# Performance work log

Hardware: AMD Instinct MI355X
Metric: run time of the kernel (lower is better)

## Reference

```python
import math
import jax, jax.numpy as jnp
import numpy as np

# dims (match init_kwargs)
N, K = 10000, 32            # nodes, padded neighbors per node
IN_F, H, HEADS = 128, 128, 8
T_F, R_F, OUT, LAYERS = 64, 32, 64, 2
HD = H // HEADS
START_T, END_T = 0.25, 0.75
ATTN_NORM = math.sqrt(1.0 / HD)
T_NORM = math.sqrt(1.0 / (T_F // 2))
EPS = 1e-5


def layernorm(x, g, b):
    m = jnp.mean(x, axis=-1, keepdims=True)
    v = jnp.var(x, axis=-1, keepdims=True)
    return (x - m) * jax.lax.rsqrt(v + EPS) * g + b


def t2v(dt, Wt, bt):
    # TimeKernel: linear(1->T_F/2) then interleaved [sin, cos] * norm
    h = dt[..., None] * Wt + bt                      # [..., T_F/2]
    return jnp.stack([jnp.sin(h), jnp.cos(h)], axis=-1).reshape(*h.shape[:-1], T_F) * T_NORM


def tgat_layer(x, neighbors, times, rels, mask,
               Wkqv, Wt, bt, Wtime, Wedge, g1, b1n, g2, b2n, W1, bl1, W2, bl2):
    xn = layernorm(x, g1, b1n)
    kqv = xn @ Wkqv                                  # [N, 3H], chunk order (k, q, v)
    k_, q_, v_ = jnp.split(kqv, 3, axis=1)
    kn = k_[neighbors]                               # [N, K, H] irregular gather
    vn = v_[neighbors]
    # per-node time reference: max over [start_t; masked times] (times>=start_t so start_t covered)
    tmax = jnp.max(jnp.where(mask, times, START_T), axis=1)        # [N]
    tq_emb = t2v(tmax - START_T, Wt, bt)             # [N, T_F] (the prepended start_t row)
    tn_emb = t2v(tmax[:, None] - times, Wt, bt)      # [N, K, T_F]
    t_qq = (tq_emb @ Wtime)[:, H:2 * H]              # query chunk of time KQV
    tkn = tn_emb @ Wtime                             # [N, K, 3H]
    re = rels @ Wedge                                # [N, K, 3H]
    q = q_ + t_qq                                    # [N, H]
    k = kn + tkn[..., :H] + re[..., :H]
    v = vn + tkn[..., 2 * H:] + re[..., 2 * H:]
    qh = q.reshape(N, HEADS, HD)
    kh = k.reshape(N, K, HEADS, HD)
    vh = v.reshape(N, K, HEADS, HD)
    scores = jnp.einsum('nhd,nkhd->nhk', qh, kh) * ATTN_NORM
    scores = jnp.where(mask[:, None, :], scores, -1e30)
    attn = jax.nn.softmax(scores, axis=-1)
    out = jnp.einsum('nhk,nkhd->nhd', attn, vh).reshape(N, H)
    has = jnp.any(mask, axis=1)                      # nodes with zero valid neighbors -> zeros
    h = jnp.where(has[:, None], out, 0.0)
    h2 = h + xn
    hn = layernorm(h2, g2, b2n)
    z = jnp.concatenate([xn, hn], axis=1)
    z = jax.nn.relu(z @ W1 + bl1) @ W2 + bl2
    return z + h2


def setup_inputs() -> dict:
    key = jax.random.key(0)
    ks = jax.random.split(key, 16)
    w = lambda i, *shape: jax.random.normal(ks[i], shape, dtype=jnp.float32) * 0.05
    return {
        'x': jax.random.normal(ks[0], (N, IN_F), dtype=jnp.float32),
        'neighbors': jax.random.randint(ks[1], (N, K), 0, N, dtype=jnp.int32),
        'times': jax.random.uniform(ks[2], (N, K), dtype=jnp.float32),
        'rels': jax.random.normal(ks[3], (N, K, R_F), dtype=jnp.float32),
        'Wp': w(4, IN_F, H), 'bp': jnp.zeros((H,), jnp.float32),
        'Wkqv': w(5, H, 3 * H),
        'Wt': w(6, T_F // 2), 'bt': jnp.zeros((T_F // 2,), jnp.float32),
        'Wtime': w(7, T_F, 3 * H),
        'Wedge': w(8, R_F, 3 * H),
        'g1': jnp.ones((H,), jnp.float32), 'b1n': jnp.zeros((H,), jnp.float32),
        'g2': jnp.ones((H,), jnp.float32), 'b2n': jnp.zeros((H,), jnp.float32),
        'W1': w(9, 2 * H, H), 'bl1': jnp.zeros((H,), jnp.float32),
        'W2': w(10, H, H), 'bl2': jnp.zeros((H,), jnp.float32),
        'Wo': w(11, H, OUT), 'bo': jnp.zeros((OUT,), jnp.float32),
    }


def reference(x, neighbors, times, rels, Wp, bp, Wkqv, Wt, bt, Wtime, Wedge,
              g1, b1n, g2, b2n, W1, bl1, W2, bl2, Wo, bo):
    mask = (times >= START_T) & (times < END_T)      # [N, K] temporal neighbor mask
    h = jax.nn.relu(x @ Wp + bp)
    for _ in range(LAYERS):                          # layers SHARE weights (ModuleList([layer]*layers))
        h = tgat_layer(h, neighbors, times, rels, mask,
                       Wkqv, Wt, bt, Wtime, Wedge, g1, b1n, g2, b2n, W1, bl1, W2, bl2)
    return h @ Wo + bo
```

## Files before the change

kernel.cpp:

```cpp
#include <hip/hip_runtime.h>
#include <hip/hip_bf16.h>

#define NN 10000
#define KK 32
#define HH 128
#define TFH 32
#define RFE 32
#define OUTF 64
#define START_T 0.25f
#define END_T 0.75f
#define ATTN_NORM 0.25f
#define T_NORM 0.17677669529663687f
#define LN_EPS 1e-5f
#define MT 64

typedef __attribute__((ext_vector_type(4))) float f32x4;
typedef __attribute__((ext_vector_type(8))) short bf16x8;

__device__ __forceinline__ ushort f2bf(float x){
  __hip_bfloat16 b = __float2bfloat16(x);
  return *(ushort*)&b;
}
__device__ __forceinline__ float bf2f(ushort u){
  __hip_bfloat16 b = *(__hip_bfloat16*)&u;
  return __bfloat162float(b);
}

__device__ __forceinline__ float groupsum32(float v){
  v += __shfl_xor(v, 16, 32);
  v += __shfl_xor(v, 8, 32);
  v += __shfl_xor(v, 4, 32);
  v += __shfl_xor(v, 2, 32);
  v += __shfl_xor(v, 1, 32);
  return v;
}

__device__ __forceinline__ float wavesum64(float v){
  v += __shfl_xor(v, 32, 64);
  v += __shfl_xor(v, 16, 64);
  v += __shfl_xor(v, 8, 64);
  v += __shfl_xor(v, 4, 64);
  v += __shfl_xor(v, 2, 64);
  v += __shfl_xor(v, 1, 64);
  return v;
}

__global__ __launch_bounds__(256) void k_prep_wT(const float* __restrict__ Wp, const float* __restrict__ Wkqv,
    const float* __restrict__ W1, const float* __restrict__ W2, const float* __restrict__ Wo,
    const float* __restrict__ Wtime, const float* __restrict__ Wedge,
    ushort* __restrict__ WpT, ushort* __restrict__ WkqvT, ushort* __restrict__ W1T,
    ushort* __restrict__ W2T, ushort* __restrict__ WoT, ushort* __restrict__ WcT){
  int id = blockIdx.x*256 + threadIdx.x;
  if (id < 16384){ int n=id>>7, k=id&127; WpT[id]=f2bf(Wp[k*HH+n]); return; }
  id -= 16384;
  if (id < 49152){ int n=id>>7, k=id&127; WkqvT[id]=f2bf(Wkqv[k*384+n]); return; }
  id -= 49152;
  if (id < 32768){ int n=id>>8, k=id&255; W1T[id]=f2bf(W1[k*HH+n]); return; }
  id -= 32768;
  if (id < 16384){ int n=id>>7, k=id&127; W2T[id]=f2bf(W2[k*HH+n]); return; }
  id -= 16384;
  if (id < 8192){ int n=id>>7, k=id&127; WoT[id]=f2bf(Wo[k*OUTF+n]); return; }
  id -= 8192;
  if (id < 24576){
    const int c = id/96, r = id%96;
    const int cc = (c < 128) ? c : (c + 128);
    const float v = (r < 64) ? Wtime[r*384 + cc] : Wedge[(r-64)*384 + cc];
    WcT[c*96 + r] = f2bf(v);
  }
}

#define LDA1 136
__global__ __launch_bounds__(256) void k_proj_mfma(const float* __restrict__ X, const ushort* __restrict__ WpT,
                                                   const float* __restrict__ bp, float* __restrict__ Y){
  __shared__ ushort As[16*LDA1];
  const int tid = threadIdx.x, n0 = blockIdx.x*16;
  #pragma unroll
  for (int p=0;p<2;++p){
    const int idx = tid + p*256;
    const int row = idx>>5, c4 = (idx&31)*4;
    const float4 v = *(const float4*)&X[(size_t)(n0+row)*HH + c4];
    *(ushort4*)&As[row*LDA1 + c4] = make_ushort4(f2bf(v.x), f2bf(v.y), f2bf(v.z), f2bf(v.w));
  }
  __syncthreads();
  const int w = tid>>6, lane = tid&63;
  const int lr = lane&15, lk8 = (lane>>4)*8, rbase = (lane>>4)*4;
  bf16x8 a[4];
  #pragma unroll
  for (int kk=0;kk<4;kk++) a[kk] = *(const bf16x8*)&As[lr*LDA1 + kk*32 + lk8];
  f32x4 acc[2];
  #pragma unroll
  for (int nt=0;nt<2;nt++) acc[nt] = (f32x4){0.f,0.f,0.f,0.f};
  #pragma unroll
  for (int nt=0;nt<2;nt++){
    const int n = w*2 + nt;
    #pragma unroll
    for (int kk=0;kk<4;kk++){
      bf16x8 b = *(const bf16x8*)&WpT[(n*16+lr)*HH + kk*32 + lk8];
      acc[nt] = __builtin_amdgcn_mfma_f32_16x16x32_bf16(a[kk], b, acc[nt],0,0,0);
    }
  }
  #pragma unroll
  for (int nt=0;nt<2;nt++){
    const int c = (w*2+nt)*16 + lr;
    const float bj = bp[c];
    #pragma unroll
    for (int r=0;r<4;r++)
      Y[(size_t)(n0 + rbase + r)*HH + c] = fmaxf(acc[nt][r] + bj, 0.f);
  }
}

__global__ __launch_bounds__(128) void k_prep_node(const float* __restrict__ times, const float* __restrict__ Wt,
                                                   const float* __restrict__ bt, const float* __restrict__ Wtime,
                                                   const int* __restrict__ nbrs,
                                                   float* __restrict__ tqq, float* __restrict__ tmaxb,
                                                   int* __restrict__ cntb, uint* __restrict__ vmaskb,
                                                   int* __restrict__ nbrC){
  __shared__ float temb[2*TFH];
  __shared__ float tm_sh;
  const int n = blockIdx.x, j = threadIdx.x;
  if (j < KK){
    float t = times[n*KK + j];
    bool valid = (t >= START_T) && (t < END_T);
    float val = valid ? t : START_T;
    #pragma unroll
    for (int off=16; off; off>>=1) val = fmaxf(val, __shfl_xor(val, off, 32));
    if (j==0){ tm_sh = val; tmaxb[n] = val; }
    const uint vm = (uint)__ballot(valid);
    if (valid){
      const int slot = __popc(vm & ((1u<<j)-1));
      nbrC[n*KK + slot] = nbrs[n*KK + j];
    }
    if (j==0){ cntb[n] = __popc(vm); vmaskb[n] = vm; }
  }
  __syncthreads();
  if (j < TFH){
    float hh = fmaf(tm_sh - START_T, Wt[j], bt[j]);
    temb[2*j]   = __sinf(hh)*T_NORM;
    temb[2*j+1] = __cosf(hh)*T_NORM;
  }
  __syncthreads();
  float acc = 0.f;
  #pragma unroll
  for (int f=0; f<2*TFH; f++) acc = fmaf(temb[f], Wtime[f*384 + HH + j], acc);
  tqq[n*HH + j] = acc;
}

#define LDA 104
#define LDKV 264
__global__ __launch_bounds__(256) void k_prep_kv4(
    const float* __restrict__ times, const float* __restrict__ rels, const float* __restrict__ tmaxb,
    const float* __restrict__ Wt, const float* __restrict__ bt, const ushort* __restrict__ WcT,
    const uint* __restrict__ vmaskb, uint4* __restrict__ kvout){
  __shared__ ushort smem[MT*LDKV];
  __shared__ float dt_sh[MT];
  ushort* Fa = smem;
  ushort* kvs = smem;
  const int tid = threadIdx.x;
  const int node0 = blockIdx.x*2;
  if (tid < MT){
    const int node = node0 + (tid>>5);
    dt_sh[tid] = tmaxb[node] - times[node*KK + (tid&31)];
  }
  __syncthreads();
  #pragma unroll
  for (int s0=0; s0<8; ++s0){
    const int s = tid + s0*256;
    const int p = s>>5, f = s&31;
    const float hh = fmaf(dt_sh[p], Wt[f], bt[f]);
    ushort2 pk;
    pk.x = f2bf(__sinf(hh)*T_NORM);
    pk.y = f2bf(__cosf(hh)*T_NORM);
    *(ushort2*)&Fa[p*LDA + 2*f] = pk;
  }
  #pragma unroll
  for (int s0=0; s0<2; ++s0){
    const int i = tid + s0*256;
    const int p = i>>3, seg = i&7;
    const float4 rv = *(const float4*)&rels[((size_t)node0*KK + p)*RFE + seg*4];
    ushort4 w2; w2.x=f2bf(rv.x); w2.y=f2bf(rv.y); w2.z=f2bf(rv.z); w2.w=f2bf(rv.w);
    *(ushort4*)&Fa[p*LDA + 64 + seg*4] = w2;
  }
  __syncthreads();
  const int wave = tid>>6, lane = tid&63;
  const int lr = lane&15, lk = (lane>>4)*8;
  f32x4 acc[4][4];
  #pragma unroll
  for (int m=0;m<4;m++)
    #pragma unroll
    for (int n=0;n<4;n++) acc[m][n] = (f32x4){0.f,0.f,0.f,0.f};
  #pragma unroll
  for (int kk=0; kk<3; ++kk){
    const int k0 = kk*32;
    bf16x8 a[4], b[4];
    #pragma unroll
    for (int m=0;m<4;m++) a[m] = *(const bf16x8*)&Fa[(m*16 + lr)*LDA + k0 + lk];
    #pragma unroll
    for (int n=0;n<4;n++) b[n] = *(const bf16x8*)&WcT[(wave*64 + n*16 + lr)*96 + k0 + lk];
    #pragma unroll
    for (int m=0;m<4;m++)
      #pragma unroll
      for (int n=0;n<4;n++)
        acc[m][n] = __builtin_amdgcn_mfma_f32_16x16x32_bf16(a[m], b[n], acc[m][n], 0,0,0);
  }
  __syncthreads();
  const int rbase = (lane>>4)*4;
  #pragma unroll
  for (int n=0;n<4;n++){
    const int c = wave*64 + n*16 + lr;
    const int ip = (c < 128) ? (2*c) : (2*(c-128)+1);
    #pragma unroll
    for (int m=0;m<4;m++)
      #pragma unroll
      for (int r=0;r<4;r++)
        kvs[(m*16 + rbase + r)*LDKV + ip] = f2bf(acc[m][n][r]);
  }
  __syncthreads();
  const uint vm0 = vmaskb[node0], vm1 = vmaskb[node0+1];
  #pragma unroll
  for (int pass=0; pass<8; ++pass){
    const int idx = pass*256 + tid;
    const int row = idx>>5, seg = idx&31;
    const int nloc = row>>5, k = row&31;
    const uint vm = nloc ? vm1 : vm0;
    if ((vm>>k)&1u){
      const int slot = __popc(vm & ((1u<<k)-1));
      const uint4 v = *(const uint4*)&kvs[row*LDKV + seg*8];
      kvout[((size_t)(node0+nloc)*KK + slot)*32 + seg] = v;
    }
  }
}

__global__ __launch_bounds__(256) void k_ln_kqv_mfma(const float* __restrict__ Hin, const ushort* __restrict__ WkqvT,
    const float* __restrict__ g1, const float* __restrict__ b1, const float* __restrict__ tqq,
    float* __restrict__ XN, ushort* __restrict__ xnb,
    float* __restrict__ Qf, ushort* __restrict__ KVb){
  __shared__ ushort As[16*LDA1];
  const int tid = threadIdx.x, n0 = blockIdx.x*16;
  const int grp = tid>>5, gl = tid&31;
  {
    const float4 gv = *(const float4*)&g1[gl*4];
    const float4 bv = *(const float4*)&b1[gl*4];
    #pragma unroll
    for (int rr=0; rr<2; ++rr){
      const int row = grp + rr*8;
      const int node = n0 + row;
      float4 hv = *(const float4*)&Hin[(size_t)node*HH + gl*4];
      float s = hv.x+hv.y+hv.z+hv.w;
      s = groupsum32(s);
      const float mean = s*(1.f/HH);
      const float dx=hv.x-mean, dy=hv.y-mean, dz=hv.z-mean, dw=hv.w-mean;
      float vs = dx*dx+dy*dy+dz*dz+dw*dw;
      vs = groupsum32(vs);
      const float rstd = rsqrtf(vs*(1.f/HH)+LN_EPS);
      const float x0=dx*rstd*gv.x+bv.x, x1=dy*rstd*gv.y+bv.y, x2=dz*rstd*gv.z+bv.z, x3=dw*rstd*gv.w+bv.w;
      ushort4 pk = make_ushort4(f2bf(x0), f2bf(x1), f2bf(x2), f2bf(x3));
      *(ushort4*)&As[row*LDA1 + gl*4] = pk;
      *(float4*)&XN[(size_t)node*HH + gl*4] = make_float4(x0,x1,x2,x3);
      *(ushort4*)&xnb[(size_t)node*HH + gl*4] = pk;
    }
  }
  __syncthreads();
  const int w = tid>>6, lane = tid&63;
  const int lr = lane&15, lk8 = (lane>>4)*8, rbase = (lane>>4)*4;
  bf16x8 a[4];
  #pragma unroll
  for (int kk=0;kk<4;kk++) a[kk] = *(const bf16x8*)&As[lr*LDA1 + kk*32 + lk8];
  f32x4 acc[6];
  #pragma unroll
  for (int nt=0;nt<6;nt++) acc[nt] = (f32x4){0.f,0.f,0.f,0.f};
  #pragma unroll
  for (int nt=0;nt<6;nt++){
    const int n = w*6 + nt;
    #pragma unroll
    for (int kk=0;kk<4;kk++){
      bf16x8 b = *(const bf16x8*)&WkqvT[(n*16+lr)*HH + kk*32 + lk8];
      acc[nt] = __builtin_amdgcn_mfma_f32_16x16x32_bf16(a[kk], b, acc[nt],0,0,0);
    }
  }
  #pragma unroll
  for (int nt=0;nt<6;nt++){
    const int c = (w*6+nt)*16 + lr;
    #pragma unroll
    for (int r=0;r<4;r++){
      const int node = n0 + rbase + r;
      const float v = acc[nt][r];
      if (c < HH)           KVb[(size_t)node*256 + 2*c] = f2bf(v);
      else if (c < 2*HH)    Qf[(size_t)node*HH + (c-HH)] = v + tqq[(size_t)node*HH + (c-HH)];
      else                  KVb[(size_t)node*256 + 2*(c-2*HH) + 1] = f2bf(v);
    }
  }
}

__global__ __launch_bounds__(256) void k_attn6(
    const float* __restrict__ Qf, const uint2* __restrict__ KVu2, const uint2* __restrict__ kvaddC2,
    const int* __restrict__ nbrC, const int* __restrict__ cntb,
    const float* __restrict__ XN, const float* __restrict__ g2, const float* __restrict__ b2,
    float* __restrict__ H2, ushort* __restrict__ hnb){
  __shared__ int nbr_sh[4][KK];
  const int tid = threadIdx.x, node0 = blockIdx.x*4;
  if (tid < 128) nbr_sh[tid>>5][tid&31] = nbrC[(node0 + (tid>>5))*KK + (tid&31)];
  __syncthreads();
  const int wv = tid>>6, l = tid&63;
  const int node = node0 + wv;
  const int cnt = cntb[node];
  const float2 q2 = *(const float2*)&Qf[(size_t)node*HH + 2*l];
  const float q0s = q2.x * ATTN_NORM, q1s = q2.y * ATTN_NORM;
  const uint2* karow = kvaddC2 + (size_t)node*KK*64 + l;
  float m_ = -3.0e38f, sume = 0.f, a0 = 0.f, a1 = 0.f;
  const int cc = (cnt + 7) >> 3;
  for (int ch=0; ch<cc; ++ch){
    const int base = ch*8;
    uint2 ka[8], kb[8];
    #pragma unroll
    for (int i=0;i<8;i++){
      int slot = base + i; slot = (slot < cnt) ? slot : (cnt-1);
      ka[i] = karow[(size_t)slot*64];
      kb[i] = KVu2[(size_t)nbr_sh[wv][slot]*64 + l];
    }
    float s[8];
    #pragma unroll
    for (int i=0;i<8;i++){
      float p = q0s * (bf2f((ushort)(kb[i].x&0xffff)) + bf2f((ushort)(ka[i].x&0xffff)))
              + q1s * (bf2f((ushort)(kb[i].y&0xffff)) + bf2f((ushort)(ka[i].y&0xffff)));
      p += __shfl_xor(p, 4, 8);
      p += __shfl_xor(p, 2, 8);
      p += __shfl_xor(p, 1, 8);
      s[i] = (base + i < cnt) ? p : -1e30f;
    }
    float cm = s[0];
    #pragma unroll
    for (int i=1;i<8;i++) cm = fmaxf(cm, s[i]);
    const float mn = fmaxf(m_, cm);
    const float sc = __expf(m_ - mn);
    sume *= sc; a0 *= sc; a1 *= sc;
    #pragma unroll
    for (int i=0;i<8;i++){
      const float e = __expf(s[i] - mn);
      sume += e;
      a0 = fmaf(e, bf2f((ushort)(kb[i].x>>16)) + bf2f((ushort)(ka[i].x>>16)), a0);
      a1 = fmaf(e, bf2f((ushort)(kb[i].y>>16)) + bf2f((ushort)(ka[i].y>>16)), a1);
    }
    m_ = mn;
  }
  const float inv = (cnt > 0) ? (1.f / sume) : 0.f;
  const float2 xn2 = *(const float2*)&XN[(size_t)node*HH + 2*l];
  const float h0 = a0*inv + xn2.x;
  const float h1 = a1*inv + xn2.y;
  *(float2*)&H2[(size_t)node*HH + 2*l] = make_float2(h0, h1);
  const float mean = wavesum64(h0 + h1) * (1.f/HH);
  const float d0 = h0 - mean, d1 = h1 - mean;
  const float var = wavesum64(d0*d0 + d1*d1) * (1.f/HH);
  const float rstd = rsqrtf(var + LN_EPS);
  const float2 gv = *(const float2*)&g2[2*l];
  const float2 bv = *(const float2*)&b2[2*l];
  ushort2 hn;
  hn.x = f2bf(d0*rstd*gv.x + bv.x);
  hn.y = f2bf(d1*rstd*gv.y + bv.y);
  *(ushort2*)&hnb[(size_t)node*HH + 2*l] = hn;
}

#define LDA2 264
template<int LAST>
__global__ __launch_bounds__(256) void k_ffn_mfma(const ushort* __restrict__ xnb, const ushort* __restrict__ hnb,
    const float* __restrict__ H2, const ushort* __restrict__ W1T, const float* __restrict__ bl1,
    const ushort* __restrict__ W2T, const float* __restrict__ bl2, float* __restrict__ HOUT,
    const ushort* __restrict__ WoT, const float* __restrict__ bo, float* __restrict__ OUT){
  __shared__ ushort As[16*LDA2];
  __shared__ ushort Ms[16*LDA1];
  const int tid = threadIdx.x, n0 = blockIdx.x*16;
  {
    const int row = tid>>4, c8 = (tid&15)*8;
    *(uint4*)&As[row*LDA2 + c8]       = *(const uint4*)&xnb[(size_t)(n0+row)*HH + c8];
    *(uint4*)&As[row*LDA2 + 128 + c8] = *(const uint4*)&hnb[(size_t)(n0+row)*HH + c8];
  }
  __syncthreads();
  const int w = tid>>6, lane = tid&63;
  const int lr = lane&15, lk8 = (lane>>4)*8, rbase = (lane>>4)*4;
  {
    bf16x8 a[8];
    #pragma unroll
    for (int kk=0;kk<8;kk++) a[kk] = *(const bf16x8*)&As[lr*LDA2 + kk*32 + lk8];
    f32x4 acc[2];
    #pragma unroll
    for (int nt=0;nt<2;nt++) acc[nt] = (f32x4){0.f,0.f,0.f,0.f};
    #pragma unroll
    for (int nt=0;nt<2;nt++){
      const int n = w*2 + nt;
      #pragma unroll
      for (int kk=0;kk<8;kk++){
        bf16x8 b = *(const bf16x8*)&W1T[(n*16+lr)*256 + kk*32 + lk8];
        acc[nt] = __builtin_amdgcn_mfma_f32_16x16x32_bf16(a[kk], b, acc[nt],0,0,0);
      }
    }
    #pragma unroll
    for (int nt=0;nt<2;nt++){
      const int c = (w*2+nt)*16 + lr;
      const float bj = bl1[c];
      #pragma unroll
      for (int r=0;r<4;r++)
        Ms[(rbase+r)*LDA1 + c] = f2bf(fmaxf(acc[nt][r] + bj, 0.f));
    }
  }
  __syncthreads();
  {
    bf16x8 a[4];
    #pragma unroll
    for (int kk=0;kk<4;kk++) a[kk] = *(const bf16x8*)&Ms[lr*LDA1 + kk*32 + lk8];
    f32x4 acc[2];
    #pragma unroll
    for (int nt=0;nt<2;nt++) acc[nt] = (f32x4){0.f,0.f,0.f,0.f};
    #pragma unroll
    for (int nt=0;nt<2;nt++){
      const int n = w*2 + nt;
      #pragma unroll
      for (int kk=0;kk<4;kk++){
        bf16x8 b = *(const bf16x8*)&W2T[(n*16+lr)*HH + kk*32 + lk8];
        acc[nt] = __builtin_amdgcn_mfma_f32_16x16x32_bf16(a[kk], b, acc[nt],0,0,0);
      }
    }
    #pragma unroll
    for (int nt=0;nt<2;nt++){
      const int c = (w*2+nt)*16 + lr;
      const float bj = bl2[c];
      #pragma unroll
      for (int r=0;r<4;r++){
        const size_t node = n0 + rbase + r;
        const float hout = acc[nt][r] + bj + H2[node*HH + c];
        if (LAST){
          ((ushort*)As)[(rbase+r)*LDA1 + c] = f2bf(hout);
        } else {
          HOUT[node*HH + c] = hout;
        }
      }
    }
  }
  if (LAST){
    __syncthreads();
    bf16x8 a[4];
    #pragma unroll
    for (int kk=0;kk<4;kk++) a[kk] = *(const bf16x8*)&((ushort*)As)[lr*LDA1 + kk*32 + lk8];
    f32x4 acc = (f32x4){0.f,0.f,0.f,0.f};
    #pragma unroll
    for (int kk=0;kk<4;kk++){
      bf16x8 b = *(const bf16x8*)&WoT[(w*16+lr)*HH + kk*32 + lk8];
      acc = __builtin_amdgcn_mfma_f32_16x16x32_bf16(a[kk], b, acc,0,0,0);
    }
    const int c = w*16 + lr;
    const float bj = bo[c];
    #pragma unroll
    for (int r=0;r<4;r++)
      OUT[(size_t)(n0 + rbase + r)*OUTF + c] = acc[r] + bj;
  }
}

extern "C" void kernel_launch(void* const* d_in, const int* in_sizes, int n_in,
                              void* d_out, int out_size, void* d_ws, size_t ws_size,
                              hipStream_t stream){
  const float* x         = (const float*)d_in[0];
  const int*   neighbors = (const int*)  d_in[1];
  const float* times     = (const float*)d_in[2];
  const float* rels      = (const float*)d_in[3];
  const float* Wp        = (const float*)d_in[4];
  const float* bp        = (const float*)d_in[5];
  const float* Wkqv      = (const float*)d_in[6];
  const float* Wt        = (const float*)d_in[7];
  const float* bt        = (const float*)d_in[8];
  const float* Wtime     = (const float*)d_in[9];
  const float* Wedge     = (const float*)d_in[10];
  const float* g1        = (const float*)d_in[11];
  const float* b1n       = (const float*)d_in[12];
  const float* g2        = (const float*)d_in[13];
  const float* b2n       = (const float*)d_in[14];
  const float* W1        = (const float*)d_in[15];
  const float* bl1       = (const float*)d_in[16];
  const float* W2        = (const float*)d_in[17];
  const float* bl2       = (const float*)d_in[18];
  const float* Wo        = (const float*)d_in[19];
  const float* bo        = (const float*)d_in[20];
  float* out = (float*)d_out;

  char* ws = (char*)d_ws;
  size_t off = 0;
  auto carve = [&](size_t bytes)->char*{
    char* p = ws + off; off = (off + bytes + 255) & ~(size_t)255; return p;
  };
  float* hA    = (float*)carve((size_t)NN*HH*4);
  float* hB    = (float*)carve((size_t)NN*HH*4);
  float* xn    = (float*)carve((size_t)NN*HH*4);
  float* h2    = (float*)carve((size_t)NN*HH*4);
  float* tqq   = (float*)carve((size_t)NN*HH*4);
  float* Qfp   = (float*)carve((size_t)NN*HH*4);
  float* tmaxb = (float*)carve((size_t)NN*4);
  int*   cntb  = (int*)carve((size_t)NN*4);
  uint*  vmaskb= (uint*)carve((size_t)NN*4);
  int*   nbrC  = (int*)carve((size_t)(NN+4)*KK*4);
  ushort* KVb  = (ushort*)carve((size_t)NN*256*2);
  ushort* xnb  = (ushort*)carve((size_t)NN*HH*2);
  ushort* hnb  = (ushort*)carve((size_t)NN*HH*2);
  ushort* WcTg = (ushort*)carve((size_t)256*96*2);
  ushort* WpT  = (ushort*)carve((size_t)16384*2);
  ushort* WkqvT= (ushort*)carve((size_t)49152*2);
  ushort* W1T  = (ushort*)carve((size_t)32768*2);
  ushort* W2T  = (ushort*)carve((size_t)16384*2);
  ushort* WoT  = (ushort*)carve((size_t)8192*2);
  uint*   kvaddC = (uint*)carve((size_t)NN*KK*256*2);
  (void)ws_size;

  k_prep_wT<<<576, 256, 0, stream>>>(Wp, Wkqv, W1, W2, Wo, Wtime, Wedge,
                                     WpT, WkqvT, W1T, W2T, WoT, WcTg);
  k_proj_mfma<<<NN/16, 256, 0, stream>>>(x, WpT, bp, hA);
  k_prep_node<<<NN, 128, 0, stream>>>(times, Wt, bt, Wtime, neighbors,
                                      tqq, tmaxb, cntb, vmaskb, nbrC);
  k_prep_kv4<<<NN/2, 256, 0, stream>>>(times, rels, tmaxb, Wt, bt, WcTg, vmaskb, (uint4*)kvaddC);

  float* cur = hA; float* nxt = hB;
  for (int layer=0; layer<2; ++layer){
    k_ln_kqv_mfma<<<NN/16, 256, 0, stream>>>(cur, WkqvT, g1, b1n, tqq, xn, xnb, Qfp, KVb);
    k_attn6<<<NN/4, 256, 0, stream>>>(Qfp, (const uint2*)KVb, (const uint2*)kvaddC, nbrC, cntb,
                                      xn, g2, b2n, h2, hnb);
    if (layer == 0)
      k_ffn_mfma<0><<<NN/16, 256, 0, stream>>>(xnb, hnb, h2, W1T, bl1, W2T, bl2, nxt,
                                               WoT, bo, out);
    else
      k_ffn_mfma<1><<<NN/16, 256, 0, stream>>>(xnb, hnb, h2, W1T, bl1, W2T, bl2, nxt,
                                               WoT, bo, out);
    float* t = cur; cur = nxt; nxt = t;
  }
}
```

Measured before the change: 176.1 us.

## Merge independent prep kernels into heterogeneous blocks to cut launches

Combines the input projection and per-node time/mask prep into one launch, with the block index choosing the role. It also runs the layer-0 layernorm+KQV work in the same launch as the neighbour time/edge KV precompute. The layer loop is unrolled so layer 0 uses the fused kernel. This removes two kernel launches and the idle gaps between small kernels. In exchange, the mixed block roles share one shared-memory footprint and register budget, which may lower occupancy for the lighter branch.

```diff
diff --git a/kernel.cpp b/kernel.cpp
--- a/kernel.cpp
+++ b/kernel.cpp
@@ -70,162 +70,232 @@
 }
 
 #define LDA1 136
-__global__ __launch_bounds__(256) void k_proj_mfma(const float* __restrict__ X, const ushort* __restrict__ WpT,
-                                                   const float* __restrict__ bp, float* __restrict__ Y){
-  __shared__ ushort As[16*LDA1];
-  const int tid = threadIdx.x, n0 = blockIdx.x*16;
-  #pragma unroll
-  for (int p=0;p<2;++p){
-    const int idx = tid + p*256;
-    const int row = idx>>5, c4 = (idx&31)*4;
-    const float4 v = *(const float4*)&X[(size_t)(n0+row)*HH + c4];
-    *(ushort4*)&As[row*LDA1 + c4] = make_ushort4(f2bf(v.x), f2bf(v.y), f2bf(v.z), f2bf(v.w));
-  }
-  __syncthreads();
-  const int w = tid>>6, lane = tid&63;
-  const int lr = lane&15, lk8 = (lane>>4)*8, rbase = (lane>>4)*4;
-  bf16x8 a[4];
-  #pragma unroll
-  for (int kk=0;kk<4;kk++) a[kk] = *(const bf16x8*)&As[lr*LDA1 + kk*32 + lk8];
-  f32x4 acc[2];
-  #pragma unroll
-  for (int nt=0;nt<2;nt++) acc[nt] = (f32x4){0.f,0.f,0.f,0.f};
-  #pragma unroll
-  for (int nt=0;nt<2;nt++){
-    const int n = w*2 + nt;
-    #pragma unroll
-    for (int kk=0;kk<4;kk++){
-      bf16x8 b = *(const bf16x8*)&WpT[(n*16+lr)*HH + kk*32 + lk8];
-      acc[nt] = __builtin_amdgcn_mfma_f32_16x16x32_bf16(a[kk], b, acc[nt],0,0,0);
-    }
-  }
-  #pragma unroll
-  for (int nt=0;nt<2;nt++){
-    const int c = (w*2+nt)*16 + lr;
-    const float bj = bp[c];
-    #pragma unroll
-    for (int r=0;r<4;r++)
-      Y[(size_t)(n0 + rbase + r)*HH + c] = fmaxf(acc[nt][r] + bj, 0.f);
-  }
-}
-
-__global__ __launch_bounds__(128) void k_prep_node(const float* __restrict__ times, const float* __restrict__ Wt,
-                                                   const float* __restrict__ bt, const float* __restrict__ Wtime,
-                                                   const int* __restrict__ nbrs,
-                                                   float* __restrict__ tqq, float* __restrict__ tmaxb,
-                                                   int* __restrict__ cntb, uint* __restrict__ vmaskb,
-                                                   int* __restrict__ nbrC){
-  __shared__ float temb[2*TFH];
-  __shared__ float tm_sh;
-  const int n = blockIdx.x, j = threadIdx.x;
-  if (j < KK){
-    float t = times[n*KK + j];
-    bool valid = (t >= START_T) && (t < END_T);
-    float val = valid ? t : START_T;
-    #pragma unroll
-    for (int off=16; off; off>>=1) val = fmaxf(val, __shfl_xor(val, off, 32));
-    if (j==0){ tm_sh = val; tmaxb[n] = val; }
-    const uint vm = (uint)__ballot(valid);
-    if (valid){
-      const int slot = __popc(vm & ((1u<<j)-1));
-      nbrC[n*KK + slot] = nbrs[n*KK + j];
-    }
-    if (j==0){ cntb[n] = __popc(vm); vmaskb[n] = vm; }
-  }
-  __syncthreads();
-  if (j < TFH){
-    float hh = fmaf(tm_sh - START_T, Wt[j], bt[j]);
-    temb[2*j]   = __sinf(hh)*T_NORM;
-    temb[2*j+1] = __cosf(hh)*T_NORM;
-  }
-  __syncthreads();
-  float acc = 0.f;
-  #pragma unroll
-  for (int f=0; f<2*TFH; f++) acc = fmaf(temb[f], Wtime[f*384 + HH + j], acc);
-  tqq[n*HH + j] = acc;
-}
-
 #define LDA 104
 #define LDKV 264
-__global__ __launch_bounds__(256) void k_prep_kv4(
+
+__global__ __launch_bounds__(256) void k_node_proj(
+    const float* __restrict__ X, const ushort* __restrict__ WpT, const float* __restrict__ bp,
+    float* __restrict__ Y,
+    const float* __restrict__ times, const int* __restrict__ nbrs,
+    const float* __restrict__ Wt, const float* __restrict__ bt, const float* __restrict__ Wtime,
+    float* __restrict__ tqq, float* __restrict__ tmaxb,
+    int* __restrict__ cntb, uint* __restrict__ vmaskb, int* __restrict__ nbrC){
+  __shared__ ushort As[16*LDA1];
+  __shared__ float temb2[2][2*TFH];
+  __shared__ float tmax_sh[2];
+  const int tid = threadIdx.x;
+  if (blockIdx.x < NN/16){
+    const int n0 = blockIdx.x*16;
+    #pragma unroll
+    for (int p=0;p<2;++p){
+      const int idx = tid + p*256;
+      const int row = idx>>5, c4 = (idx&31)*4;
+      const float4 v = *(const float4*)&X[(size_t)(n0+row)*HH + c4];
+      *(ushort4*)&As[row*LDA1 + c4] = make_ushort4(f2bf(v.x), f2bf(v.y), f2bf(v.z), f2bf(v.w));
+    }
+    __syncthreads();
+    const int w = tid>>6, lane = tid&63;
+    const int lr = lane&15, lk8 = (lane>>4)*8, rbase = (lane>>4)*4;
+    bf16x8 a[4];
+    #pragma unroll
+    for (int kk=0;kk<4;kk++) a[kk] = *(const bf16x8*)&As[lr*LDA1 + kk*32 + lk8];
+    f32x4 acc[2];
+    #pragma unroll
+    for (int nt=0;nt<2;nt++) acc[nt] = (f32x4){0.f,0.f,0.f,0.f};
+    #pragma unroll
+    for (int nt=0;nt<2;nt++){
+      const int n = w*2 + nt;
+      #pragma unroll
+      for (int kk=0;kk<4;kk++){
+        bf16x8 b = *(const bf16x8*)&WpT[(n*16+lr)*HH + kk*32 + lk8];
+        acc[nt] = __builtin_amdgcn_mfma_f32_16x16x32_bf16(a[kk], b, acc[nt],0,0,0);
+      }
+    }
+    #pragma unroll
+    for (int nt=0;nt<2;nt++){
+      const int c = (w*2+nt)*16 + lr;
+      const float bj = bp[c];
+      #pragma unroll
+      for (int r=0;r<4;r++)
+        Y[(size_t)(n0 + rbase + r)*HH + c] = fmaxf(acc[nt][r] + bj, 0.f);
+    }
+  } else {
+    const int node0 = (blockIdx.x - NN/16)*2;
+    if (tid < MT){
+      const int i = tid>>5, k = tid&31;
+      const int node = node0 + i;
+      const float t = times[node*KK + k];
+      const bool valid = (t >= START_T) && (t < END_T);
+      float val = valid ? t : START_T;
+      #pragma unroll
+      for (int off=16; off; off>>=1) val = fmaxf(val, __shfl_xor(val, off, 32));
+      const unsigned long long bal = __ballot(valid);
+      const uint vm = (uint)(bal >> (i*32));
+      if (valid){
+        const int slot = __popc(vm & ((1u<<k)-1));
+        nbrC[node*KK + slot] = nbrs[node*KK + k];
+      }
+      if (k==0){ cntb[node] = __popc(vm); vmaskb[node] = vm; tmaxb[node] = val; tmax_sh[i] = val; }
+    }
+    __syncthreads();
+    if (tid < MT){
+      const int i = tid>>5, f = tid&31;
+      const float hh = fmaf(tmax_sh[i] - START_T, Wt[f], bt[f]);
+      temb2[i][2*f]   = __sinf(hh)*T_NORM;
+      temb2[i][2*f+1] = __cosf(hh)*T_NORM;
+    }
+    __syncthreads();
+    {
+      const int i = tid>>7, jj = tid&127;
+      float acc = 0.f;
+      #pragma unroll
+      for (int f=0; f<2*TFH; f++) acc = fmaf(temb2[i][f], Wtime[f*384 + HH + jj], acc);
+      tqq[(size_t)(node0+i)*HH + jj] = acc;
+    }
+  }
+}
+
+__global__ __launch_bounds__(256) void k_kv0_ln0(
     const float* __restrict__ times, const float* __restrict__ rels, const float* __restrict__ tmaxb,
     const float* __restrict__ Wt, const float* __restrict__ bt, const ushort* __restrict__ WcT,
-    const uint* __restrict__ vmaskb, uint4* __restrict__ kvout){
+    const uint* __restrict__ vmaskb, uint4* __restrict__ kvout,
+    const float* __restrict__ Hin, const ushort* __restrict__ WkqvT,
+    const float* __restrict__ g1, const float* __restrict__ b1, const float* __restrict__ tqq,
+    float* __restrict__ XN, ushort* __restrict__ xnb,
+    float* __restrict__ Qf, ushort* __restrict__ KVb){
   __shared__ ushort smem[MT*LDKV];
   __shared__ float dt_sh[MT];
-  ushort* Fa = smem;
-  ushort* kvs = smem;
   const int tid = threadIdx.x;
-  const int node0 = blockIdx.x*2;
-  if (tid < MT){
-    const int node = node0 + (tid>>5);
-    dt_sh[tid] = tmaxb[node] - times[node*KK + (tid&31)];
-  }
-  __syncthreads();
-  #pragma unroll
-  for (int s0=0; s0<8; ++s0){
-    const int s = tid + s0*256;
-    const int p = s>>5, f = s&31;
-    const float hh = fmaf(dt_sh[p], Wt[f], bt[f]);
-    ushort2 pk;
-    pk.x = f2bf(__sinf(hh)*T_NORM);
-    pk.y = f2bf(__cosf(hh)*T_NORM);
-    *(ushort2*)&Fa[p*LDA + 2*f] = pk;
-  }
-  #pragma unroll
-  for (int s0=0; s0<2; ++s0){
-    const int i = tid + s0*256;
-    const int p = i>>3, seg = i&7;
-    const float4 rv = *(const float4*)&rels[((size_t)node0*KK + p)*RFE + seg*4];
-    ushort4 w2; w2.x=f2bf(rv.x); w2.y=f2bf(rv.y); w2.z=f2bf(rv.z); w2.w=f2bf(rv.w);
-    *(ushort4*)&Fa[p*LDA + 64 + seg*4] = w2;
-  }
-  __syncthreads();
-  const int wave = tid>>6, lane = tid&63;
-  const int lr = lane&15, lk = (lane>>4)*8;
-  f32x4 acc[4][4];
-  #pragma unroll
-  for (int m=0;m<4;m++)
-    #pragma unroll
-    for (int n=0;n<4;n++) acc[m][n] = (f32x4){0.f,0.f,0.f,0.f};
-  #pragma unroll
-  for (int kk=0; kk<3; ++kk){
-    const int k0 = kk*32;
-    bf16x8 a[4], b[4];
-    #pragma unroll
-    for (int m=0;m<4;m++) a[m] = *(const bf16x8*)&Fa[(m*16 + lr)*LDA + k0 + lk];
-    #pragma unroll
-    for (int n=0;n<4;n++) b[n] = *(const bf16x8*)&WcT[(wave*64 + n*16 + lr)*96 + k0 + lk];
+  if (blockIdx.x < NN/16){
+    ushort* As = smem;
+    const int n0 = blockIdx.x*16;
+    const int grp = tid>>5, gl = tid&31;
+    {
+      const float4 gv = *(const float4*)&g1[gl*4];
+      const float4 bv = *(const float4*)&b1[gl*4];
+      #pragma unroll
+      for (int rr=0; rr<2; ++rr){
+        const int row = grp + rr*8;
+        const int node = n0 + row;
+        float4 hv = *(const float4*)&Hin[(size_t)node*HH + gl*4];
+        float s = hv.x+hv.y+hv.z+hv.w;
+        s = groupsum32(s);
+        const float mean = s*(1.f/HH);
+        const float dx=hv.x-mean, dy=hv.y-mean, dz=hv.z-mean, dw=hv.w-mean;
+        float vs = dx*dx+dy*dy+dz*dz+dw*dw;
+        vs = groupsum32(vs);
+        const float rstd = rsqrtf(vs*(1.f/HH)+LN_EPS);
+        const float x0=dx*rstd*gv.x+bv.x, x1=dy*rstd*gv.y+bv.y, x2=dz*rstd*gv.z+bv.z, x3=dw*rstd*gv.w+bv.w;
+        ushort4 pk = make_ushort4(f2bf(x0), f2bf(x1), f2bf(x2), f2bf(x3));
+        *(ushort4*)&As[row*LDA1 + gl*4] = pk;
+        *(float4*)&XN[(size_t)node*HH + gl*4] = make_float4(x0,x1,x2,x3);
+        *(ushort4*)&xnb[(size_t)node*HH + gl*4] = pk;
+      }
+    }
+    __syncthreads();
+    const int w = tid>>6, lane = tid&63;
+    const int lr = lane&15, lk8 = (lane>>4)*8, rbase = (lane>>4)*4;
+    bf16x8 a[4];
+    #pragma unroll
+    for (int kk=0;kk<4;kk++) a[kk] = *(const bf16x8*)&As[lr*LDA1 + kk*32 + lk8];
+    f32x4 acc[6];
+    #pragma unroll
+    for (int nt=0;nt<6;nt++) acc[nt] = (f32x4){0.f,0.f,0.f,0.f};
+    #pragma unroll
+    for (int nt=0;nt<6;nt++){
+      const int n = w*6 + nt;
+      #pragma unroll
+      for (int kk=0;kk<4;kk++){
+        bf16x8 b = *(const bf16x8*)&WkqvT[(n*16+lr)*HH + kk*32 + lk8];
+        acc[nt] = __builtin_amdgcn_mfma_f32_16x16x32_bf16(a[kk], b, acc[nt],0,0,0);
+      }
+    }
+    #pragma unroll
+    for (int nt=0;nt<6;nt++){
+      const int c = (w*6+nt)*16 + lr;
+      #pragma unroll
+      for (int r=0;r<4;r++){
+        const int node = n0 + rbase + r;
+        const float v = acc[nt][r];
+        if (c < HH)           KVb[(size_t)node*256 + 2*c] = f2bf(v);
+        else if (c < 2*HH)    Qf[(size_t)node*HH + (c-HH)] = v + tqq[(size_t)node*HH + (c-HH)];
+        else                  KVb[(size_t)node*256 + 2*(c-2*HH) + 1] = f2bf(v);
+      }
+    }
+  } else {
+    ushort* Fa = smem;
+    ushort* kvs = smem;
+    const int node0 = (blockIdx.x - NN/16)*2;
+    if (tid < MT){
+      const int node = node0 + (tid>>5);
+      dt_sh[tid] = tmaxb[node] - times[node*KK + (tid&31)];
+    }
+    __syncthreads();
+    #pragma unroll
+    for (int s0=0; s0<8; ++s0){
+      const int s = tid + s0*256;
+      const int p = s>>5, f = s&31;
+      const float hh = fmaf(dt_sh[p], Wt[f], bt[f]);
+      ushort2 pk;
+      pk.x = f2bf(__sinf(hh)*T_NORM);
+      pk.y = f2bf(__cosf(hh)*T_NORM);
+      *(ushort2*)&Fa[p*LDA + 2*f] = pk;
+    }
+    #pragma unroll
+    for (int s0=0; s0<2; ++s0){
+      const int i = tid + s0*256;
+      const int p = i>>3, seg = i&7;
+      const float4 rv = *(const float4*)&rels[((size_t)node0*KK + p)*RFE + seg*4];
+      ushort4 w2; w2.x=f2bf(rv.x); w2.y=f2bf(rv.y); w2.z=f2bf(rv.z); w2.w=f2bf(rv.w);
+      *(ushort4*)&Fa[p*LDA + 64 + seg*4] = w2;
+    }
+    __syncthreads();
+    const int wave = tid>>6, lane = tid&63;
+    const int lr = lane&15, lk = (lane>>4)*8;
+    f32x4 acc[4][4];
     #pragma unroll
     for (int m=0;m<4;m++)
       #pragma unroll
-      for (int n=0;n<4;n++)
-        acc[m][n] = __builtin_amdgcn_mfma_f32_16x16x32_bf16(a[m], b[n], acc[m][n], 0,0,0);
-  }
-  __syncthreads();
-  const int rbase = (lane>>4)*4;
-  #pragma unroll
-  for (int n=0;n<4;n++){
-    const int c = wave*64 + n*16 + lr;
-    const int ip = (c < 128) ? (2*c) : (2*(c-128)+1);
-    #pragma unroll
-    for (int m=0;m<4;m++)
-      #pragma unroll
-      for (int r=0;r<4;r++)
-        kvs[(m*16 + rbase + r)*LDKV + ip] = f2bf(acc[m][n][r]);
-  }
-  __syncthreads();
-  const uint vm0 = vmaskb[node0], vm1 = vmaskb[node0+1];
-  #pragma unroll
-  for (int pass=0; pass<8; ++pass){
-    const int idx = pass*256 + tid;
-    const int row = idx>>5, seg = idx&31;
-    const int nloc = row>>5, k = row&31;
-    const uint vm = nloc ? vm1 : vm0;
-    if ((vm>>k)&1u){
-      const int slot = __popc(vm & ((1u<<k)-1));
-      const uint4 v = *(const uint4*)&kvs[row*LDKV + seg*8];
-      kvout[((size_t)(node0+nloc)*KK + slot)*32 + seg] = v;
+      for (int n=0;n<4;n++) acc[m][n] = (f32x4){0.f,0.f,0.f,0.f};
+    #pragma unroll
+    for (int kk=0; kk<3; ++kk){
+      const int k0 = kk*32;
+      bf16x8 a[4], b[4];
+      #pragma unroll
+      for (int m=0;m<4;m++) a[m] = *(const bf16x8*)&Fa[(m*16 + lr)*LDA + k0 + lk];
+      #pragma unroll
+      for (int n=0;n<4;n++) b[n] = *(const bf16x8*)&WcT[(wave*64 + n*16 + lr)*96 + k0 + lk];
+      #pragma unroll
+      for (int m=0;m<4;m++)
+        #pragma unroll
+        for (int n=0;n<4;n++)
+          acc[m][n] = __builtin_amdgcn_mfma_f32_16x16x32_bf16(a[m], b[n], acc[m][n], 0,0,0);
+    }
+    __syncthreads();
+    const int rbase = (lane>>4)*4;
+    #pragma unroll
+    for (int n=0;n<4;n++){
+      const int c = wave*64 + n*16 + lr;
+      const int ip = (c < 128) ? (2*c) : (2*(c-128)+1);
+      #pragma unroll
+      for (int m=0;m<4;m++)
+        #pragma unroll
+        for (int r=0;r<4;r++)
+          kvs[(m*16 + rbase + r)*LDKV + ip] = f2bf(acc[m][n][r]);
+    }
+    __syncthreads();
+    const uint vm0 = vmaskb[node0], vm1 = vmaskb[node0+1];
+    #pragma unroll
+    for (int pass=0; pass<8; ++pass){
+      const int idx = pass*256 + tid;
+      const int row = idx>>5, seg = idx&31;
+      const int nloc = row>>5, k = row&31;
+      const uint vm = nloc ? vm1 : vm0;
+      if ((vm>>k)&1u){
+        const int slot = __popc(vm & ((1u<<k)-1));
+        const uint4 v = *(const uint4*)&kvs[row*LDKV + seg*8];
+        kvout[((size_t)(node0+nloc)*KK + slot)*32 + seg] = v;
+      }
     }
   }
 }
@@ -508,22 +578,19 @@
 
   k_prep_wT<<<576, 256, 0, stream>>>(Wp, Wkqv, W1, W2, Wo, Wtime, Wedge,
                                      WpT, WkqvT, W1T, W2T, WoT, WcTg);
-  k_proj_mfma<<<NN/16, 256, 0, stream>>>(x, WpT, bp, hA);
-  k_prep_node<<<NN, 128, 0, stream>>>(times, Wt, bt, Wtime, neighbors,
-                                      tqq, tmaxb, cntb, vmaskb, nbrC);
-  k_prep_kv4<<<NN/2, 256, 0, stream>>>(times, rels, tmaxb, Wt, bt, WcTg, vmaskb, (uint4*)kvaddC);
-
-  float* cur = hA; float* nxt = hB;
-  for (int layer=0; layer<2; ++layer){
-    k_ln_kqv_mfma<<<NN/16, 256, 0, stream>>>(cur, WkqvT, g1, b1n, tqq, xn, xnb, Qfp, KVb);
-    k_attn6<<<NN/4, 256, 0, stream>>>(Qfp, (const uint2*)KVb, (const uint2*)kvaddC, nbrC, cntb,
-                                      xn, g2, b2n, h2, hnb);
-    if (layer == 0)
-      k_ffn_mfma<0><<<NN/16, 256, 0, stream>>>(xnb, hnb, h2, W1T, bl1, W2T, bl2, nxt,
-                                               WoT, bo, out);
-    else
-      k_ffn_mfma<1><<<NN/16, 256, 0, stream>>>(xnb, hnb, h2, W1T, bl1, W2T, bl2, nxt,
-                                               WoT, bo, out);
-    float* t = cur; cur = nxt; nxt = t;
-  }
-}
+  k_node_proj<<<NN/16 + NN/2, 256, 0, stream>>>(x, WpT, bp, hA,
+                                                times, neighbors, Wt, bt, Wtime,
+                                                tqq, tmaxb, cntb, vmaskb, nbrC);
+  k_kv0_ln0<<<NN/16 + NN/2, 256, 0, stream>>>(times, rels, tmaxb, Wt, bt, WcTg, vmaskb,
+                                              (uint4*)kvaddC,
+                                              hA, WkqvT, g1, b1n, tqq, xn, xnb, Qfp, KVb);
+  k_attn6<<<NN/4, 256, 0, stream>>>(Qfp, (const uint2*)KVb, (const uint2*)kvaddC, nbrC, cntb,
+                                    xn, g2, b2n, h2, hnb);
+  k_ffn_mfma<0><<<NN/16, 256, 0, stream>>>(xnb, hnb, h2, W1T, bl1, W2T, bl2, hB,
+                                           WoT, bo, out);
+  k_ln_kqv_mfma<<<NN/16, 256, 0, stream>>>(hB, WkqvT, g1, b1n, tqq, xn, xnb, Qfp, KVb);
+  k_attn6<<<NN/4, 256, 0, stream>>>(Qfp, (const uint2*)KVb, (const uint2*)kvaddC, nbrC, cntb,
+                                    xn, g2, b2n, h2, hnb);
+  k_ffn_mfma<1><<<NN/16, 256, 0, stream>>>(xnb, hnb, h2, W1T, bl1, W2T, bl2, hA,
+                                           WoT, bo, out);
+}
```

Result: faster. 165.5 us (-6.0%).
